# Kernel optimization log

Measured on AMD Instinct MI355X. Metric: run time of the kernel, lower is better.

## Reference

```python
import jax, jax.numpy as jnp
import numpy as np

NUM_LABELS_I = 28  # 7 entity types * 4 (B/I/E/S)
NUM_LABELS = 31    # + O, EOS, BOS
INDEX_O, INDEX_EOS, INDEX_BOS = 28, 29, 30
NEG = -10000.0


def _make_trans(rng):
    # replicate ChainCRF4NestedNER.reset_parameters() structural masking
    bs = np.arange(0, NUM_LABELS_I, 4)
    is_ = bs + 1
    es = bs + 2
    ss = bs + 3
    t = (rng.standard_normal((NUM_LABELS, NUM_LABELS)) * 0.1).astype(np.float32)
    for i in bs:
        t[i, :i + 1] = NEG; t[i, i + 3:] = NEG
    for i in is_:
        t[i, :i] = NEG; t[i, i + 2:] = NEG
    for i in np.concatenate([es, ss, [INDEX_O]]):
        t[i, is_] = NEG; t[i, es] = NEG; t[i, INDEX_BOS] = NEG
    t[INDEX_EOS, :INDEX_EOS] = NEG; t[INDEX_EOS, INDEX_BOS] = NEG
    t[INDEX_BOS, is_] = NEG; t[INDEX_BOS, es] = NEG; t[INDEX_BOS, INDEX_BOS] = NEG
    return jnp.asarray(t)


def setup_inputs() -> dict:
    B, T, D = 64, 512, 768
    key = jax.random.key(0)
    k1, k2, k3 = jax.random.split(key, 3)
    inp = jax.random.normal(k1, (B, T, D), dtype=jnp.float32)
    target = jax.random.randint(k2, (B, T), 0, 29, dtype=jnp.int64)  # real labels + O only
    mask = jnp.ones((B, T), dtype=jnp.float32)
    state_w = jax.random.normal(k3, (NUM_LABELS, D), dtype=jnp.float32) * 0.02
    state_b = jnp.concatenate([jnp.zeros(INDEX_EOS, jnp.float32),
                               jnp.full(NUM_LABELS - INDEX_EOS, NEG, jnp.float32)])
    trans = _make_trans(np.random.default_rng(0))
    return {"input": inp, "target": target, "mask": mask,
            "state_w": state_w, "state_b": state_b, "trans": trans}


def reference(input, target, mask, state_w, state_b, trans):
    B, T, _ = input.shape
    # state scores [B, T, L]
    out_s = jnp.einsum('btd,ld->btl', input, state_w) + state_b
    out_s = out_s.at[:, :, INDEX_EOS].add((mask == 0).astype(out_s.dtype) * 20000.0)
    # energy [B, T, L, L]: trans[prev, curr] + state[curr]
    energy = trans[None, None, :, :] + out_s[:, :, None, :]
    # forward algorithm (logsumexp semiring) as a scan over time
    energy_t = jnp.moveaxis(energy, 1, 0)  # [T, B, L, L]
    part0 = energy_t[0, :, INDEX_BOS, :]   # [B, L]

    def step(part, e_t):
        new = jax.nn.logsumexp(e_t + part[:, :, None], axis=1)
        return new, None

    partition, _ = jax.lax.scan(step, part0, energy_t[1:])
    # gold-path energy: sum_t energy[b, t, prev_label, label]
    prev = jnp.concatenate([jnp.full((B, 1), INDEX_BOS, dtype=target.dtype),
                            target[:, :-1]], axis=1)
    bi = jnp.arange(B)[:, None]
    ti = jnp.arange(T)[None, :]
    tgt_energy = energy[bi, ti, prev, target].sum(axis=1)
    loss = jax.nn.logsumexp(trans[:, INDEX_EOS][None, :] + partition, axis=1) - tgt_energy
    return loss, energy
```

## Files before the change

### kernel.cpp

```cpp
#include <hip/hip_runtime.h>

typedef float f32x4  __attribute__((ext_vector_type(4)));
typedef float f32x16 __attribute__((ext_vector_type(16)));
typedef short s16x8  __attribute__((ext_vector_type(8)));

constexpr int NL  = 31;
constexpr int BB  = 64;
constexpr int TT  = 512;
constexpr int DD  = 768;
constexpr int RTOT = BB * TT;
constexpr int IDX_EOS = 29;
constexpr int IDX_BOS = 30;
constexpr float LOG2E = 1.4426950408889634f;
constexpr float LN2F  = 0.6931471805599453f;

union Frag8 { unsigned u[4]; s16x8 s; };

__device__ inline unsigned pk2(float a, float b) {
  unsigned ua = __float_as_uint(a), ub = __float_as_uint(b);
  ua = (ua + 0x7fffu + ((ua >> 16) & 1u)) >> 16;
  ub = (ub + 0x7fffu + ((ub >> 16) & 1u)) >> 16;
  return ua | (ub << 16);
}
__device__ inline unsigned short bf16r(float a) {
  unsigned ua = __float_as_uint(a);
  return (unsigned short)((ua + 0x7fffu + ((ua >> 16) & 1u)) >> 16);
}

__device__ inline float bfly_max32(float v) {
#define STEPM(K) { float o = __int_as_float(__builtin_amdgcn_ds_swizzle(__float_as_int(v), ((K) << 10) | 0x1f)); v = fmaxf(v, o); }
  STEPM(1) STEPM(2) STEPM(4) STEPM(8) STEPM(16)
#undef STEPM
  return v;
}
__device__ inline float bfly_sum32(float v) {
#define STEPS(K) { float o = __int_as_float(__builtin_amdgcn_ds_swizzle(__float_as_int(v), ((K) << 10) | 0x1f)); v = v + o; }
  STEPS(1) STEPS(2) STEPS(4) STEPS(8) STEPS(16)
#undef STEPS
  return v;
}

__device__ inline void repack(const float E[16], int h, Frag8& B1, Frag8& B2) {
  unsigned o1a = pk2(E[4 * h], E[4 * h + 1]), o1b = pk2(E[4 * h + 2], E[4 * h + 3]);
  unsigned o2a = pk2(E[8 + 4 * h], E[8 + 4 * h + 1]), o2b = pk2(E[8 + 4 * h + 2], E[8 + 4 * h + 3]);
  int hb = 4 * (1 - h);
  unsigned s1a = pk2(E[hb], E[hb + 1]),         s1b = pk2(E[hb + 2], E[hb + 3]);
  unsigned s2a = pk2(E[8 + hb], E[8 + hb + 1]), s2b = pk2(E[8 + hb + 2], E[8 + hb + 3]);
  unsigned r1a = __shfl_xor((int)s1a, 32), r1b = __shfl_xor((int)s1b, 32);
  unsigned r2a = __shfl_xor((int)s2a, 32), r2b = __shfl_xor((int)s2b, 32);
  if (h == 0) {
    B1.u[0] = o1a; B1.u[1] = o1b; B1.u[2] = r1a; B1.u[3] = r1b;
    B2.u[0] = o2a; B2.u[1] = o2b; B2.u[2] = r2a; B2.u[3] = r2b;
  } else {
    B1.u[0] = r1a; B1.u[1] = r1b; B1.u[2] = o1a; B1.u[3] = o1b;
    B2.u[0] = r2a; B2.u[1] = r2b; B2.u[2] = o2a; B2.u[3] = o2b;
  }
}

__device__ inline float renorm16(float E[16], float& Sacc) {
  float m = E[0];
#pragma unroll
  for (int r = 1; r < 16; ++r) m = fmaxf(m, E[r]);
  m = bfly_max32(m);
  m = fmaxf(m, __shfl_xor(m, 32));
  float lg = truncf(log2f(m));
  Sacc += lg;
  float sc = exp2f(-lg);
#pragma unroll
  for (int r = 0; r < 16; ++r) E[r] *= sc;
  return m;
}

__device__ inline void load_A(const float* M, int l, int h, Frag8& A1, Frag8& A2) {
  const float* row = M + (l & 31) * 32 + 8 * h;
  f32x4 a = *(const f32x4*)(row);
  f32x4 b = *(const f32x4*)(row + 4);
  f32x4 c = *(const f32x4*)(row + 16);
  f32x4 d = *(const f32x4*)(row + 20);
  A1.u[0] = pk2(a[0], a[1]); A1.u[1] = pk2(a[2], a[3]);
  A1.u[2] = pk2(b[0], b[1]); A1.u[3] = pk2(b[2], b[3]);
  A2.u[0] = pk2(c[0], c[1]); A2.u[1] = pk2(c[2], c[3]);
  A2.u[2] = pk2(d[0], d[1]); A2.u[3] = pk2(d[2], d[3]);
}

__device__ inline void load_B(const float* M, int l, int h, Frag8& B1, Frag8& B2) {
  int nn = l & 31;
#pragma unroll
  for (int m = 0; m < 4; ++m) {
    int k = 8 * h + 2 * m;
    B1.u[m] = pk2(M[k * 32 + nn],        M[(k + 1) * 32 + nn]);
    B2.u[m] = pk2(M[(k + 16) * 32 + nn], M[(k + 17) * 32 + nn]);
  }
}

__global__ void k_prep(const float* __restrict__ sw, unsigned short* __restrict__ Bw) {
  for (int i = blockIdx.x * 256 + threadIdx.x; i < 32 * DD; i += 8 * 256)
    Bw[i] = (i < NL * DD) ? bf16r(sw[i]) : (unsigned short)0;
}

__global__ __launch_bounds__(256) void k_outs(
    const float* __restrict__ inp, const unsigned short* __restrict__ Bw,
    const float* __restrict__ sb, const float* __restrict__ msk,
    float* __restrict__ outs)
{
  __shared__ unsigned short As[2][64 * 72];
  int tid = threadIdx.x, wave = tid >> 6, lane = tid & 63;
  int quad = lane >> 4, l15 = lane & 15;
  int r0 = blockIdx.x * 64;
  int lrow = tid >> 4;
  const float* gsrc = inp + (size_t)r0 * DD + (tid & 15) * 4;

  f32x4 pre[4];
#pragma unroll
  for (int p = 0; p < 4; ++p)
    pre[p] = *(const f32x4*)(gsrc + (size_t)(p * 16 + lrow) * DD);

  f32x4 acc[2] = {};
  for (int kc = 0; kc < 12; ++kc) {
    unsigned* dstb = (unsigned*)As[kc & 1];
#pragma unroll
    for (int p = 0; p < 4; ++p) {
      int row = p * 16 + lrow;
      dstb[row * 36 + (tid & 15) * 2]     = pk2(pre[p][0], pre[p][1]);
      dstb[row * 36 + (tid & 15) * 2 + 1] = pk2(pre[p][2], pre[p][3]);
    }
    __syncthreads();
    if (kc < 11) {
      const float* g2 = gsrc + (kc + 1) * 64;
#pragma unroll
      for (int p = 0; p < 4; ++p)
        pre[p] = *(const f32x4*)(g2 + (size_t)(p * 16 + lrow) * DD);
    }
    const unsigned short* asb = As[kc & 1];
#pragma unroll
    for (int ks = 0; ks < 2; ++ks) {
      s16x8 af = *(const s16x8*)(asb + (wave * 16 + l15) * 72 + ks * 32 + quad * 8);
#pragma unroll
      for (int ct = 0; ct < 2; ++ct) {
        s16x8 bf = *(const s16x8*)(Bw + (ct * 16 + l15) * DD + kc * 64 + ks * 32 + quad * 8);
        acc[ct] = __builtin_amdgcn_mfma_f32_16x16x32_bf16(af, bf, acc[ct], 0, 0, 0);
      }
    }
    __syncthreads();
  }
#pragma unroll
  for (int ct = 0; ct < 2; ++ct) {
    int n = ct * 16 + l15;
    if (n >= NL) continue;
    float b = sb[n];
#pragma unroll
    for (int r = 0; r < 4; ++r) {
      int row = r0 + wave * 16 + quad * 4 + r;
      float v = acc[ct][r] + b;
      if (n == IDX_EOS && msk[row] == 0.f) v += 20000.f;
      outs[(size_t)row * NL + n] = v;
    }
  }
}

__global__ __launch_bounds__(256) void k_seg(
    const float* __restrict__ outs, const float* __restrict__ trans,
    float* __restrict__ Mseg, float* __restrict__ Sseg)
{
  __shared__ float Ub[4][8 * 32];
  int tid = threadIdx.x, wave = tid >> 6, lane = tid & 63;
  int l = lane & 31, h = lane >> 5;
  int unit = blockIdx.x * 4 + wave;
  int b = unit >> 6, c = unit & 63;
  int t0 = 1 + c * 8;
  int n = (c == 63) ? 7 : 8;

  float* ub = Ub[wave];
#pragma unroll
  for (int it = 0; it < 4; ++it) {
    int idx = lane + it * 64;
    int row = idx >> 5, col = idx & 31;
    float v = 0.f;
    if (col < NL && row < n)
      v = exp2f(LOG2E * outs[((size_t)b * TT + t0 + row) * NL + col]);
    ub[idx] = v;
  }
  __syncthreads();

  Frag8 A1, A2, B1, B2;
#pragma unroll
  for (int m = 0; m < 4; ++m) {
    int k0 = 8 * h + 2 * m, k1 = k0 + 1;
    float a0 = (k0 < NL && l < NL) ? exp2f(LOG2E * trans[k0 * NL + l]) : 0.f;
    float a1 = (k1 < NL && l < NL) ? exp2f(LOG2E * trans[k1 * NL + l]) : 0.f;
    A1.u[m] = pk2(a0, a1);
    int k2 = 16 + k0, k3 = 16 + k1;
    float a2 = (k2 < NL && l < NL) ? exp2f(LOG2E * trans[k2 * NL + l]) : 0.f;
    float a3 = (k3 < NL && l < NL) ? exp2f(LOG2E * trans[k3 * NL + l]) : 0.f;
    A2.u[m] = pk2(a2, a3);
    B1.u[m] = ((k0 == l) ? 0x3f80u : 0u) | (((k1 == l) ? 0x3f80u : 0u) << 16);
    B2.u[m] = ((k2 == l) ? 0x3f80u : 0u) | (((k3 == l) ? 0x3f80u : 0u) << 16);
  }

  float E[16];
  for (int s = 0; s < n; ++s) {
    const float* us = ub + s * 32 + 4 * h;
    f32x4 u0 = *(const f32x4*)(us);
    f32x4 u1 = *(const f32x4*)(us + 8);
    f32x4 u2 = *(const f32x4*)(us + 16);
    f32x4 u3 = *(const f32x4*)(us + 24);
    f32x16 D = {};
    D = __builtin_amdgcn_mfma_f32_32x32x16_bf16(A1.s, B1.s, D, 0, 0, 0);
    D = __builtin_amdgcn_mfma_f32_32x32x16_bf16(A2.s, B2.s, D, 0, 0, 0);
#pragma unroll
    for (int jj = 0; jj < 4; ++jj) {
      E[jj]      = D[jj]      * u0[jj];
      E[4 + jj]  = D[4 + jj]  * u1[jj];
      E[8 + jj]  = D[8 + jj]  * u2[jj];
      E[12 + jj] = D[12 + jj] * u3[jj];
    }
    if (s + 1 < n) repack(E, h, B1, B2);
  }
  float S = 0.f;
  renorm16(E, S);
  float* mo = Mseg + (size_t)unit * 1024;
#pragma unroll
  for (int r = 0; r < 16; ++r) {
    int row = (r & 3) + 8 * (r >> 2) + 4 * h;
    mo[row * 32 + l] = E[r];
  }
  if (lane == 0) Sseg[unit] = S;
}

__global__ __launch_bounds__(256) void k_tree1(
    const float* __restrict__ Mseg, const float* __restrict__ Sseg,
    float* __restrict__ Mq, float* __restrict__ Sq)
{
  int tid = threadIdx.x, wave = tid >> 6, lane = tid & 63;
  int l = lane & 31, h = lane >> 5;
  int unit = blockIdx.x * 4 + wave;
  const float* base = Mseg + (size_t)unit * 4096;
  Frag8 A1, A2, B1, B2;
  load_B(base, l, h, B1, B2);
  float S = Sseg[unit * 4] + Sseg[unit * 4 + 1] + Sseg[unit * 4 + 2] + Sseg[unit * 4 + 3];
  float E[16];
#pragma unroll
  for (int i = 1; i < 4; ++i) {
    load_A(base + i * 1024, l, h, A1, A2);
    f32x16 D = {};
    D = __builtin_amdgcn_mfma_f32_32x32x16_bf16(A1.s, B1.s, D, 0, 0, 0);
    D = __builtin_amdgcn_mfma_f32_32x32x16_bf16(A2.s, B2.s, D, 0, 0, 0);
#pragma unroll
    for (int r = 0; r < 16; ++r) E[r] = D[r];
    if (i < 3) repack(E, h, B1, B2);
  }
  renorm16(E, S);
  float* mo = Mq + (size_t)unit * 1024;
#pragma unroll
  for (int r = 0; r < 16; ++r) {
    int row = (r & 3) + 8 * (r >> 2) + 4 * h;
    mo[row * 32 + l] = E[r];
  }
  if (lane == 0) Sq[unit] = S;
}

__global__ __launch_bounds__(256) void k_tree2(
    const float* __restrict__ outs, const float* __restrict__ trans,
    const float* __restrict__ Mq, const float* __restrict__ Sq,
    float* __restrict__ ws_lse)
{
  int tid = threadIdx.x, wave = tid >> 6, lane = tid & 63;
  int l = lane & 31, h = lane >> 5;
  int b = blockIdx.x * 4 + wave;
  const float* base = Mq + (size_t)b * 16384;
  Frag8 A1, A2, B1, B2;
  load_B(base, l, h, B1, B2);
  float S = 0.f;
#pragma unroll
  for (int q = 0; q < 16; ++q) S += Sq[b * 16 + q];
  float E[16];
  for (int i = 1; i < 16; ++i) {
    load_A(base + i * 1024, l, h, A1, A2);
    f32x16 D = {};
    D = __builtin_amdgcn_mfma_f32_32x32x16_bf16(A1.s, B1.s, D, 0, 0, 0);
    D = __builtin_amdgcn_mfma_f32_32x32x16_bf16(A2.s, B2.s, D, 0, 0, 0);
#pragma unroll
    for (int r = 0; r < 16; ++r) E[r] = D[r];
    if ((i & 3) == 3) renorm16(E, S);
    if (i < 15) repack(E, h, B1, B2);
  }
  float p0 = (l < NL) ? exp2f(LOG2E * (trans[IDX_BOS * NL + l] + outs[(size_t)b * TT * NL + l])) : 0.f;
  float sum_h = 0.f;
#pragma unroll
  for (int r = 0; r < 16; ++r) {
    float s = bfly_sum32(E[r] * p0);
    int row = (r & 3) + 8 * (r >> 2) + 4 * h;
    float We = (row < NL) ? exp2f(LOG2E * trans[row * NL + IDX_EOS]) : 0.f;
    sum_h += s * We;
  }
  float tot = sum_h + __shfl_xor(sum_h, 32);
  if (lane == 0) ws_lse[b] = LN2F * (S + log2f(tot));
}

__global__ __launch_bounds__(256) void k_energy(
    const float* __restrict__ outs, const float* __restrict__ trans,
    const int* __restrict__ target, float* __restrict__ energy,
    float* __restrict__ ws_tgt)
{
  __shared__ float tr[961];
  __shared__ float oshm[32 * NL];
  int r0 = blockIdx.x * 32;
  for (int idx = threadIdx.x; idx < 961; idx += 256) tr[idx] = trans[idx];
  for (int idx = threadIdx.x; idx < 32 * NL; idx += 256)
    oshm[idx] = outs[(size_t)r0 * NL + idx];
  __syncthreads();

  if (threadIdx.x < 32) {
    int r = r0 + threadIdx.x;
    int tgt = target[r];
    int prv = ((r & (TT - 1)) == 0) ? IDX_BOS : target[r - 1];
    float c = tr[prv * NL + tgt] + oshm[threadIdx.x * NL + tgt];
    for (int off = 16; off; off >>= 1) c += __shfl_down(c, off, 32);
    if (threadIdx.x == 0) atomicAdd(&ws_tgt[r0 / TT], c);
  }

  int e0 = threadIdx.x, e1 = e0 + 256, e2 = e0 + 512, e3 = e0 + 768;
  float t0 = tr[e0], t1 = tr[e1], t2 = tr[e2];
  bool w3 = (e3 < 961);
  float t3 = w3 ? tr[e3] : 0.f;
  int j0 = e0 % 31, j1 = e1 % 31, j2 = e2 % 31, j3 = e3 % 31;
  for (int rr = 0; rr < 32; ++rr) {
    const float* ob = &oshm[rr * NL];
    float* dst = energy + (size_t)(r0 + rr) * 961;
    dst[e0] = t0 + ob[j0];
    dst[e1] = t1 + ob[j1];
    dst[e2] = t2 + ob[j2];
    if (w3) dst[e3] = t3 + ob[j3];
  }
}

__global__ void k_loss(const float* __restrict__ ws_lse,
                       const float* __restrict__ ws_tgt,
                       float* __restrict__ loss)
{
  int b = threadIdx.x;
  if (b < BB) loss[b] = ws_lse[b] - ws_tgt[b];
}

extern "C" void kernel_launch(void* const* d_in, const int* in_sizes, int n_in,
                              void* d_out, int out_size, void* d_ws, size_t ws_size,
                              hipStream_t stream) {
  const float* inp   = (const float*)d_in[0];
  const int*   tgt   = (const int*)d_in[1];
  const float* msk   = (const float*)d_in[2];
  const float* sw    = (const float*)d_in[3];
  const float* sb    = (const float*)d_in[4];
  const float* trans = (const float*)d_in[5];

  float* out    = (float*)d_out;
  float* loss   = out;
  float* energy = out + BB;
  float* Mseg = energy;
  float* Mq   = energy + (size_t)4096 * 1024;
  float* Sseg = energy + (size_t)4096 * 1024 + 1024 * 1024;
  float* Sq   = Sseg + 4096;
  unsigned short* Bw = (unsigned short*)(Sq + 1024);

  float* outs   = (float*)d_ws;
  float* ws_tgt = outs + (size_t)RTOT * NL;
  float* ws_lse = ws_tgt + 64;

  hipMemsetAsync(ws_tgt, 0, 64 * sizeof(float), stream);
  k_prep<<<8, 256, 0, stream>>>(sw, Bw);
  k_outs<<<RTOT / 64, 256, 0, stream>>>(inp, Bw, sb, msk, outs);
  k_seg<<<1024, 256, 0, stream>>>(outs, trans, Mseg, Sseg);
  k_tree1<<<256, 256, 0, stream>>>(Mseg, Sseg, Mq, Sq);
  k_tree2<<<16, 256, 0, stream>>>(outs, trans, Mq, Sq, ws_lse);
  k_energy<<<RTOT / 32, 256, 0, stream>>>(outs, trans, tgt, energy, ws_tgt);
  k_loss<<<1, 64, 0, stream>>>(ws_lse, ws_tgt, loss);
}
```

Measured before the change: 328.6 us.

## Fuse segment scan with energy write, store bf16 segment matrices in workspace

The segment-product kernel and the energy-writing kernel are merged into one launch with block-index dispatch, so the small scan work overlaps the large energy store. Energy stores become vectorized float4 writes computed with magic-number division. Segment and tree matrices are kept in bf16 in workspace instead of fp32 in the energy output buffer, which halves their traffic and removes the ordering dependency on energy. The memset and the loss kernel are folded into the prep and tree2 kernels. k_outs now gives each wave its own LDS tile without block barriers. Extra bf16 rounding of the intermediate matrices may slightly change accuracy.

```diff
diff --git a/kernel.cpp b/kernel.cpp
--- a/kernel.cpp
+++ b/kernel.cpp
@@ -57,7 +57,7 @@
   }
 }
 
-__device__ inline float renorm16(float E[16], float& Sacc) {
+__device__ inline void renorm16(float E[16], float& Sacc) {
   float m = E[0];
 #pragma unroll
   for (int r = 1; r < 16; ++r) m = fmaxf(m, E[r]);
@@ -68,32 +68,26 @@
   float sc = exp2f(-lg);
 #pragma unroll
   for (int r = 0; r < 16; ++r) E[r] *= sc;
-  return m;
-}
-
-__device__ inline void load_A(const float* M, int l, int h, Frag8& A1, Frag8& A2) {
-  const float* row = M + (l & 31) * 32 + 8 * h;
-  f32x4 a = *(const f32x4*)(row);
-  f32x4 b = *(const f32x4*)(row + 4);
-  f32x4 c = *(const f32x4*)(row + 16);
-  f32x4 d = *(const f32x4*)(row + 20);
-  A1.u[0] = pk2(a[0], a[1]); A1.u[1] = pk2(a[2], a[3]);
-  A1.u[2] = pk2(b[0], b[1]); A1.u[3] = pk2(b[2], b[3]);
-  A2.u[0] = pk2(c[0], c[1]); A2.u[1] = pk2(c[2], c[3]);
-  A2.u[2] = pk2(d[0], d[1]); A2.u[3] = pk2(d[2], d[3]);
-}
-
-__device__ inline void load_B(const float* M, int l, int h, Frag8& B1, Frag8& B2) {
-  int nn = l & 31;
+}
+
+__device__ inline void load_A16(const unsigned short* M, int l, int h, Frag8& A1, Frag8& A2) {
+  A1.s = *(const s16x8*)(M + l * 32 + 8 * h);
+  A2.s = *(const s16x8*)(M + l * 32 + 16 + 8 * h);
+}
+__device__ inline void load_B16(const unsigned short* M, int l, int h, Frag8& B1, Frag8& B2) {
 #pragma unroll
   for (int m = 0; m < 4; ++m) {
     int k = 8 * h + 2 * m;
-    B1.u[m] = pk2(M[k * 32 + nn],        M[(k + 1) * 32 + nn]);
-    B2.u[m] = pk2(M[(k + 16) * 32 + nn], M[(k + 17) * 32 + nn]);
-  }
-}
-
-__global__ void k_prep(const float* __restrict__ sw, unsigned short* __restrict__ Bw) {
+    unsigned lo0 = M[k * 32 + l],        hi0 = M[(k + 1) * 32 + l];
+    unsigned lo1 = M[(k + 16) * 32 + l], hi1 = M[(k + 17) * 32 + l];
+    B1.u[m] = lo0 | (hi0 << 16);
+    B2.u[m] = lo1 | (hi1 << 16);
+  }
+}
+
+__global__ void k_prep(const float* __restrict__ sw, unsigned short* __restrict__ Bw,
+                       float* __restrict__ ws_tgt) {
+  if (blockIdx.x == 0 && threadIdx.x < BB) ws_tgt[threadIdx.x] = 0.f;
   for (int i = blockIdx.x * 256 + threadIdx.x; i < 32 * DD; i += 8 * 256)
     Bw[i] = (i < NL * DD) ? bf16r(sw[i]) : (unsigned short)0;
 }
@@ -103,45 +97,41 @@
     const float* __restrict__ sb, const float* __restrict__ msk,
     float* __restrict__ outs)
 {
-  __shared__ unsigned short As[2][64 * 72];
+  __shared__ unsigned short As[4][16 * 72];
   int tid = threadIdx.x, wave = tid >> 6, lane = tid & 63;
   int quad = lane >> 4, l15 = lane & 15;
-  int r0 = blockIdx.x * 64;
-  int lrow = tid >> 4;
-  const float* gsrc = inp + (size_t)r0 * DD + (tid & 15) * 4;
+  int r0 = blockIdx.x * 64 + wave * 16;
+  int srow = lane >> 2, scol = lane & 3;
+  const float* gsrc = inp + (size_t)(r0 + srow) * DD + scol * 4;
+  unsigned short* asb = As[wave];
+  unsigned* dw = (unsigned*)asb;
+  int wbase = srow * 36 + scol * 2;
 
   f32x4 pre[4];
 #pragma unroll
-  for (int p = 0; p < 4; ++p)
-    pre[p] = *(const f32x4*)(gsrc + (size_t)(p * 16 + lrow) * DD);
+  for (int i = 0; i < 4; ++i) pre[i] = *(const f32x4*)(gsrc + i * 16);
 
   f32x4 acc[2] = {};
   for (int kc = 0; kc < 12; ++kc) {
-    unsigned* dstb = (unsigned*)As[kc & 1];
-#pragma unroll
-    for (int p = 0; p < 4; ++p) {
-      int row = p * 16 + lrow;
-      dstb[row * 36 + (tid & 15) * 2]     = pk2(pre[p][0], pre[p][1]);
-      dstb[row * 36 + (tid & 15) * 2 + 1] = pk2(pre[p][2], pre[p][3]);
-    }
-    __syncthreads();
+#pragma unroll
+    for (int i = 0; i < 4; ++i) {
+      dw[wbase + i * 8]     = pk2(pre[i][0], pre[i][1]);
+      dw[wbase + i * 8 + 1] = pk2(pre[i][2], pre[i][3]);
+    }
     if (kc < 11) {
       const float* g2 = gsrc + (kc + 1) * 64;
 #pragma unroll
-      for (int p = 0; p < 4; ++p)
-        pre[p] = *(const f32x4*)(g2 + (size_t)(p * 16 + lrow) * DD);
-    }
-    const unsigned short* asb = As[kc & 1];
+      for (int i = 0; i < 4; ++i) pre[i] = *(const f32x4*)(g2 + i * 16);
+    }
 #pragma unroll
     for (int ks = 0; ks < 2; ++ks) {
-      s16x8 af = *(const s16x8*)(asb + (wave * 16 + l15) * 72 + ks * 32 + quad * 8);
+      s16x8 af = *(const s16x8*)(asb + l15 * 72 + ks * 32 + quad * 8);
 #pragma unroll
       for (int ct = 0; ct < 2; ++ct) {
         s16x8 bf = *(const s16x8*)(Bw + (ct * 16 + l15) * DD + kc * 64 + ks * 32 + quad * 8);
         acc[ct] = __builtin_amdgcn_mfma_f32_16x16x32_bf16(af, bf, acc[ct], 0, 0, 0);
       }
     }
-    __syncthreads();
   }
 #pragma unroll
   for (int ct = 0; ct < 2; ++ct) {
@@ -150,7 +140,7 @@
     float b = sb[n];
 #pragma unroll
     for (int r = 0; r < 4; ++r) {
-      int row = r0 + wave * 16 + quad * 4 + r;
+      int row = r0 + quad * 4 + r;
       float v = acc[ct][r] + b;
       if (n == IDX_EOS && msk[row] == 0.f) v += 20000.f;
       outs[(size_t)row * NL + n] = v;
@@ -158,90 +148,145 @@
   }
 }
 
-__global__ __launch_bounds__(256) void k_seg(
+__global__ __launch_bounds__(256) void k_main(
     const float* __restrict__ outs, const float* __restrict__ trans,
-    float* __restrict__ Mseg, float* __restrict__ Sseg)
+    const int* __restrict__ target, float* __restrict__ energy,
+    unsigned short* __restrict__ Mseg16, float* __restrict__ Sseg,
+    float* __restrict__ ws_tgt)
 {
-  __shared__ float Ub[4][8 * 32];
+  __shared__ float smem[961 + 64 * NL];
+  int bid = blockIdx.x;
   int tid = threadIdx.x, wave = tid >> 6, lane = tid & 63;
-  int l = lane & 31, h = lane >> 5;
-  int unit = blockIdx.x * 4 + wave;
-  int b = unit >> 6, c = unit & 63;
-  int t0 = 1 + c * 8;
-  int n = (c == 63) ? 7 : 8;
-
-  float* ub = Ub[wave];
-#pragma unroll
-  for (int it = 0; it < 4; ++it) {
-    int idx = lane + it * 64;
-    int row = idx >> 5, col = idx & 31;
-    float v = 0.f;
-    if (col < NL && row < n)
-      v = exp2f(LOG2E * outs[((size_t)b * TT + t0 + row) * NL + col]);
-    ub[idx] = v;
-  }
+
+  if (bid < 1024) {
+    int l = lane & 31, h = lane >> 5;
+    int unit = bid * 4 + wave;
+    int b = unit >> 6, c = unit & 63;
+    int t0 = 1 + c * 8;
+    int n = (c == 63) ? 7 : 8;
+
+    float* ub = smem + wave * 256;
+#pragma unroll
+    for (int it = 0; it < 4; ++it) {
+      int idx = lane + it * 64;
+      int row = idx >> 5, col = idx & 31;
+      float v = 0.f;
+      if (col < NL && row < n)
+        v = exp2f(LOG2E * outs[((size_t)b * TT + t0 + row) * NL + col]);
+      ub[idx] = v;
+    }
+    __syncthreads();
+
+    Frag8 A1, A2, B1, B2;
+#pragma unroll
+    for (int m = 0; m < 4; ++m) {
+      int k0 = 8 * h + 2 * m, k1 = k0 + 1;
+      float a0 = (k0 < NL && l < NL) ? exp2f(LOG2E * trans[k0 * NL + l]) : 0.f;
+      float a1 = (k1 < NL && l < NL) ? exp2f(LOG2E * trans[k1 * NL + l]) : 0.f;
+      A1.u[m] = pk2(a0, a1);
+      int k2 = 16 + k0, k3 = 16 + k1;
+      float a2 = (k2 < NL && l < NL) ? exp2f(LOG2E * trans[k2 * NL + l]) : 0.f;
+      float a3 = (k3 < NL && l < NL) ? exp2f(LOG2E * trans[k3 * NL + l]) : 0.f;
+      A2.u[m] = pk2(a2, a3);
+      B1.u[m] = ((k0 == l) ? 0x3f80u : 0u) | (((k1 == l) ? 0x3f80u : 0u) << 16);
+      B2.u[m] = ((k2 == l) ? 0x3f80u : 0u) | (((k3 == l) ? 0x3f80u : 0u) << 16);
+    }
+
+    float E[16];
+    for (int s = 0; s < n; ++s) {
+      const float* us = ub + s * 32 + 4 * h;
+      f32x4 u0 = *(const f32x4*)(us);
+      f32x4 u1 = *(const f32x4*)(us + 8);
+      f32x4 u2 = *(const f32x4*)(us + 16);
+      f32x4 u3 = *(const f32x4*)(us + 24);
+      f32x16 D = {};
+      D = __builtin_amdgcn_mfma_f32_32x32x16_bf16(A1.s, B1.s, D, 0, 0, 0);
+      D = __builtin_amdgcn_mfma_f32_32x32x16_bf16(A2.s, B2.s, D, 0, 0, 0);
+#pragma unroll
+      for (int jj = 0; jj < 4; ++jj) {
+        E[jj]      = D[jj]      * u0[jj];
+        E[4 + jj]  = D[4 + jj]  * u1[jj];
+        E[8 + jj]  = D[8 + jj]  * u2[jj];
+        E[12 + jj] = D[12 + jj] * u3[jj];
+      }
+      if (s + 1 < n) repack(E, h, B1, B2);
+    }
+    float S = 0.f;
+    renorm16(E, S);
+    unsigned short* mo = Mseg16 + (size_t)unit * 1024;
+#pragma unroll
+    for (int r = 0; r < 16; ++r) {
+      int row = (r & 3) + 8 * (r >> 2) + 4 * h;
+      mo[row * 32 + l] = bf16r(E[r]);
+    }
+    if (lane == 0) Sseg[unit] = S;
+    return;
+  }
+
+  int r0 = (bid - 1024) * 64;
+  float* tr  = smem;
+  float* osh = smem + 961;
+  for (int idx = tid; idx < 961; idx += 256) tr[idx] = trans[idx];
+  for (int idx = tid; idx < 64 * NL; idx += 256)
+    osh[idx] = outs[(size_t)r0 * NL + idx];
   __syncthreads();
 
-  Frag8 A1, A2, B1, B2;
-#pragma unroll
-  for (int m = 0; m < 4; ++m) {
-    int k0 = 8 * h + 2 * m, k1 = k0 + 1;
-    float a0 = (k0 < NL && l < NL) ? exp2f(LOG2E * trans[k0 * NL + l]) : 0.f;
-    float a1 = (k1 < NL && l < NL) ? exp2f(LOG2E * trans[k1 * NL + l]) : 0.f;
-    A1.u[m] = pk2(a0, a1);
-    int k2 = 16 + k0, k3 = 16 + k1;
-    float a2 = (k2 < NL && l < NL) ? exp2f(LOG2E * trans[k2 * NL + l]) : 0.f;
-    float a3 = (k3 < NL && l < NL) ? exp2f(LOG2E * trans[k3 * NL + l]) : 0.f;
-    A2.u[m] = pk2(a2, a3);
-    B1.u[m] = ((k0 == l) ? 0x3f80u : 0u) | (((k1 == l) ? 0x3f80u : 0u) << 16);
-    B2.u[m] = ((k2 == l) ? 0x3f80u : 0u) | (((k3 == l) ? 0x3f80u : 0u) << 16);
-  }
-
-  float E[16];
-  for (int s = 0; s < n; ++s) {
-    const float* us = ub + s * 32 + 4 * h;
-    f32x4 u0 = *(const f32x4*)(us);
-    f32x4 u1 = *(const f32x4*)(us + 8);
-    f32x4 u2 = *(const f32x4*)(us + 16);
-    f32x4 u3 = *(const f32x4*)(us + 24);
-    f32x16 D = {};
-    D = __builtin_amdgcn_mfma_f32_32x32x16_bf16(A1.s, B1.s, D, 0, 0, 0);
-    D = __builtin_amdgcn_mfma_f32_32x32x16_bf16(A2.s, B2.s, D, 0, 0, 0);
-#pragma unroll
-    for (int jj = 0; jj < 4; ++jj) {
-      E[jj]      = D[jj]      * u0[jj];
-      E[4 + jj]  = D[4 + jj]  * u1[jj];
-      E[8 + jj]  = D[8 + jj]  * u2[jj];
-      E[12 + jj] = D[12 + jj] * u3[jj];
-    }
-    if (s + 1 < n) repack(E, h, B1, B2);
-  }
-  float S = 0.f;
-  renorm16(E, S);
-  float* mo = Mseg + (size_t)unit * 1024;
-#pragma unroll
-  for (int r = 0; r < 16; ++r) {
-    int row = (r & 3) + 8 * (r >> 2) + 4 * h;
-    mo[row * 32 + l] = E[r];
-  }
-  if (lane == 0) Sseg[unit] = S;
+  if (tid < 64) {
+    int r = r0 + tid;
+    int tg = target[r];
+    int prv = ((r & (TT - 1)) == 0) ? IDX_BOS : target[r - 1];
+    float cc = tr[prv * NL + tg] + osh[tid * NL + tg];
+#pragma unroll
+    for (int off = 32; off; off >>= 1) cc += __shfl_down(cc, off);
+    if (tid == 0) atomicAdd(&ws_tgt[r0 / TT], cc);
+  }
+
+  float* dst = energy + (size_t)r0 * 961;
+#pragma unroll 4
+  for (int it = 0; it < 60; ++it) {
+    int v = it * 256 + tid;
+    int e = v * 4;
+    f32x4 val;
+#pragma unroll
+    for (int k = 0; k < 4; ++k) {
+      unsigned x = e + k;
+      unsigned q = __umulhi(x, 4469269u);
+      unsigned c = x - q * 961u;
+      unsigned j = c - 31u * ((c * 67651u) >> 21);
+      val[k] = tr[c] + osh[q * NL + j];
+    }
+    *(f32x4*)(dst + e) = val;
+  }
+  if (tid < 16) {
+    int e = (15360 + tid) * 4;
+    f32x4 val;
+#pragma unroll
+    for (int k = 0; k < 4; ++k) {
+      unsigned x = e + k;
+      unsigned q = __umulhi(x, 4469269u);
+      unsigned c = x - q * 961u;
+      unsigned j = c - 31u * ((c * 67651u) >> 21);
+      val[k] = tr[c] + osh[q * NL + j];
+    }
+    *(f32x4*)(dst + e) = val;
+  }
 }
 
 __global__ __launch_bounds__(256) void k_tree1(
-    const float* __restrict__ Mseg, const float* __restrict__ Sseg,
-    float* __restrict__ Mq, float* __restrict__ Sq)
+    const unsigned short* __restrict__ Mseg16, const float* __restrict__ Sseg,
+    unsigned short* __restrict__ Mq16, float* __restrict__ Sq)
 {
   int tid = threadIdx.x, wave = tid >> 6, lane = tid & 63;
   int l = lane & 31, h = lane >> 5;
   int unit = blockIdx.x * 4 + wave;
-  const float* base = Mseg + (size_t)unit * 4096;
+  const unsigned short* base = Mseg16 + (size_t)unit * 4096;
   Frag8 A1, A2, B1, B2;
-  load_B(base, l, h, B1, B2);
+  load_B16(base, l, h, B1, B2);
   float S = Sseg[unit * 4] + Sseg[unit * 4 + 1] + Sseg[unit * 4 + 2] + Sseg[unit * 4 + 3];
   float E[16];
 #pragma unroll
   for (int i = 1; i < 4; ++i) {
-    load_A(base + i * 1024, l, h, A1, A2);
+    load_A16(base + i * 1024, l, h, A1, A2);
     f32x16 D = {};
     D = __builtin_amdgcn_mfma_f32_32x32x16_bf16(A1.s, B1.s, D, 0, 0, 0);
     D = __builtin_amdgcn_mfma_f32_32x32x16_bf16(A2.s, B2.s, D, 0, 0, 0);
@@ -250,32 +295,32 @@
     if (i < 3) repack(E, h, B1, B2);
   }
   renorm16(E, S);
-  float* mo = Mq + (size_t)unit * 1024;
+  unsigned short* mo = Mq16 + (size_t)unit * 1024;
 #pragma unroll
   for (int r = 0; r < 16; ++r) {
     int row = (r & 3) + 8 * (r >> 2) + 4 * h;
-    mo[row * 32 + l] = E[r];
+    mo[row * 32 + l] = bf16r(E[r]);
   }
   if (lane == 0) Sq[unit] = S;
 }
 
 __global__ __launch_bounds__(256) void k_tree2(
     const float* __restrict__ outs, const float* __restrict__ trans,
-    const float* __restrict__ Mq, const float* __restrict__ Sq,
-    float* __restrict__ ws_lse)
+    const unsigned short* __restrict__ Mq16, const float* __restrict__ Sq,
+    const float* __restrict__ ws_tgt, float* __restrict__ loss)
 {
   int tid = threadIdx.x, wave = tid >> 6, lane = tid & 63;
   int l = lane & 31, h = lane >> 5;
   int b = blockIdx.x * 4 + wave;
-  const float* base = Mq + (size_t)b * 16384;
+  const unsigned short* base = Mq16 + (size_t)b * 16384;
   Frag8 A1, A2, B1, B2;
-  load_B(base, l, h, B1, B2);
+  load_B16(base, l, h, B1, B2);
   float S = 0.f;
 #pragma unroll
   for (int q = 0; q < 16; ++q) S += Sq[b * 16 + q];
   float E[16];
   for (int i = 1; i < 16; ++i) {
-    load_A(base + i * 1024, l, h, A1, A2);
+    load_A16(base + i * 1024, l, h, A1, A2);
     f32x16 D = {};
     D = __builtin_amdgcn_mfma_f32_32x32x16_bf16(A1.s, B1.s, D, 0, 0, 0);
     D = __builtin_amdgcn_mfma_f32_32x32x16_bf16(A2.s, B2.s, D, 0, 0, 0);
@@ -294,52 +339,7 @@
     sum_h += s * We;
   }
   float tot = sum_h + __shfl_xor(sum_h, 32);
-  if (lane == 0) ws_lse[b] = LN2F * (S + log2f(tot));
-}
-
-__global__ __launch_bounds__(256) void k_energy(
-    const float* __restrict__ outs, const float* __restrict__ trans,
-    const int* __restrict__ target, float* __restrict__ energy,
-    float* __restrict__ ws_tgt)
-{
-  __shared__ float tr[961];
-  __shared__ float oshm[32 * NL];
-  int r0 = blockIdx.x * 32;
-  for (int idx = threadIdx.x; idx < 961; idx += 256) tr[idx] = trans[idx];
-  for (int idx = threadIdx.x; idx < 32 * NL; idx += 256)
-    oshm[idx] = outs[(size_t)r0 * NL + idx];
-  __syncthreads();
-
-  if (threadIdx.x < 32) {
-    int r = r0 + threadIdx.x;
-    int tgt = target[r];
-    int prv = ((r & (TT - 1)) == 0) ? IDX_BOS : target[r - 1];
-    float c = tr[prv * NL + tgt] + oshm[threadIdx.x * NL + tgt];
-    for (int off = 16; off; off >>= 1) c += __shfl_down(c, off, 32);
-    if (threadIdx.x == 0) atomicAdd(&ws_tgt[r0 / TT], c);
-  }
-
-  int e0 = threadIdx.x, e1 = e0 + 256, e2 = e0 + 512, e3 = e0 + 768;
-  float t0 = tr[e0], t1 = tr[e1], t2 = tr[e2];
-  bool w3 = (e3 < 961);
-  float t3 = w3 ? tr[e3] : 0.f;
-  int j0 = e0 % 31, j1 = e1 % 31, j2 = e2 % 31, j3 = e3 % 31;
-  for (int rr = 0; rr < 32; ++rr) {
-    const float* ob = &oshm[rr * NL];
-    float* dst = energy + (size_t)(r0 + rr) * 961;
-    dst[e0] = t0 + ob[j0];
-    dst[e1] = t1 + ob[j1];
-    dst[e2] = t2 + ob[j2];
-    if (w3) dst[e3] = t3 + ob[j3];
-  }
-}
-
-__global__ void k_loss(const float* __restrict__ ws_lse,
-                       const float* __restrict__ ws_tgt,
-                       float* __restrict__ loss)
-{
-  int b = threadIdx.x;
-  if (b < BB) loss[b] = ws_lse[b] - ws_tgt[b];
+  if (lane == 0) loss[b] = LN2F * (S + log2f(tot)) - ws_tgt[b];
 }
 
 extern "C" void kernel_launch(void* const* d_in, const int* in_sizes, int n_in,
@@ -355,22 +355,18 @@
   float* out    = (float*)d_out;
   float* loss   = out;
   float* energy = out + BB;
-  float* Mseg = energy;
-  float* Mq   = energy + (size_t)4096 * 1024;
-  float* Sseg = energy + (size_t)4096 * 1024 + 1024 * 1024;
-  float* Sq   = Sseg + 4096;
-  unsigned short* Bw = (unsigned short*)(Sq + 1024);
 
   float* outs   = (float*)d_ws;
-  float* ws_tgt = outs + (size_t)RTOT * NL;
-  float* ws_lse = ws_tgt + 64;
-
-  hipMemsetAsync(ws_tgt, 0, 64 * sizeof(float), stream);
-  k_prep<<<8, 256, 0, stream>>>(sw, Bw);
+  float* Sseg   = outs + (size_t)RTOT * NL;
+  float* Sq     = Sseg + 4096;
+  float* ws_tgt = Sq + 1024;
+  unsigned short* Mseg16 = (unsigned short*)(ws_tgt + 64);
+  unsigned short* Mq16   = Mseg16 + (size_t)4096 * 1024;
+  unsigned short* Bw     = Mq16 + (size_t)1024 * 1024;
+
+  k_prep<<<8, 256, 0, stream>>>(sw, Bw, ws_tgt);
   k_outs<<<RTOT / 64, 256, 0, stream>>>(inp, Bw, sb, msk, outs);
-  k_seg<<<1024, 256, 0, stream>>>(outs, trans, Mseg, Sseg);
-  k_tree1<<<256, 256, 0, stream>>>(Mseg, Sseg, Mq, Sq);
-  k_tree2<<<16, 256, 0, stream>>>(outs, trans, Mq, Sq, ws_lse);
-  k_energy<<<RTOT / 32, 256, 0, stream>>>(outs, trans, tgt, energy, ws_tgt);
-  k_loss<<<1, 64, 0, stream>>>(ws_lse, ws_tgt, loss);
-}
+  k_main<<<1536, 256, 0, stream>>>(outs, trans, tgt, energy, Mseg16, Sseg, ws_tgt);
+  k_tree1<<<256, 256, 0, stream>>>(Mseg16, Sseg, Mq16, Sq);
+  k_tree2<<<16, 256, 0, stream>>>(outs, trans, Mq16, Sq, ws_tgt, loss);
+}
```

After: 299.8 us. -8.8%, faster.
